# Kernel tuning notes

Measured on AMD Instinct MI355X. Metric: run time of the kernel, lower is better.

## Reference

```python
import jax, jax.numpy as jnp
import numpy as np

MODEL_DIM = 1024
HEADS = 16
HEAD_DIM = MODEL_DIM // HEADS
OUT_DIM = 1024
B, S = 2, 2048


def setup_inputs() -> dict:
    key = jax.random.key(0)
    ks = jax.random.split(key, 10)
    scale = 1.0 / np.sqrt(MODEL_DIM)
    return {
        "query": jax.random.normal(ks[0], (B, S, MODEL_DIM), dtype=jnp.float32),
        "bank": jax.random.normal(ks[1], (B, S, MODEL_DIM), dtype=jnp.float32),
        "Wq": jax.random.normal(ks[2], (MODEL_DIM, MODEL_DIM), dtype=jnp.float32) * scale,
        "bq": jnp.zeros((MODEL_DIM,), dtype=jnp.float32),
        "Wk": jax.random.normal(ks[3], (MODEL_DIM, MODEL_DIM), dtype=jnp.float32) * scale,
        "bk": jnp.zeros((MODEL_DIM,), dtype=jnp.float32),
        "Wv": jax.random.normal(ks[4], (MODEL_DIM, MODEL_DIM), dtype=jnp.float32) * scale,
        "bv": jnp.zeros((MODEL_DIM,), dtype=jnp.float32),
        "Wo": jax.random.normal(ks[5], (OUT_DIM, MODEL_DIM), dtype=jnp.float32) * scale,
        "bo": jnp.zeros((OUT_DIM,), dtype=jnp.float32),
    }


def _split_heads(x):
    # [B, S, D] -> [B, H, S, hd]
    b, s, _ = x.shape
    return x.reshape(b, s, HEADS, HEAD_DIM).transpose(0, 2, 1, 3)


def reference(query, bank, Wq, bq, Wk, bk, Wv, bv, Wo, bo):
    # Linear projections (torch Linear: x @ W.T + b)
    q = _split_heads(query @ Wq.T + bq)  # [B,H,Sq,hd]
    k = _split_heads(bank @ Wk.T + bk)   # [B,H,Sk,hd]
    v = _split_heads(bank @ Wv.T + bv)   # [B,H,Sk,hd]
    score_scale = jnp.sqrt(jnp.float32(HEAD_DIM))
    scores = jnp.einsum("bhqd,bhkd->bhqk", q / score_scale, k)  # [B,H,Sq,Sk]
    attn = jax.nn.softmax(scores, axis=-1)
    # dropout is identity in eval-mode reference
    ctx = jnp.einsum("bhqk,bhkd->bhqd", attn, v)  # [B,H,Sq,hd]
    b, h, sq, hd = ctx.shape
    ctx = ctx.transpose(0, 2, 1, 3).reshape(b, sq, MODEL_DIM)
    return ctx @ Wo.T + bo
```

## Files before the change

kernel.cpp:

```cpp
#include <hip/hip_runtime.h>


#define BDIM   2
#define SDIM   2048
#define DDIM   1024
#define HEADS  16
#define HD     64
#define MROWS  (BDIM * SDIM)

typedef float  f32x4  __attribute__((ext_vector_type(4)));
typedef __bf16 bf16x8 __attribute__((ext_vector_type(8)));
typedef __bf16 bf16x4 __attribute__((ext_vector_type(4)));

#define QSCALE 0.18033688011112042f

__device__ __forceinline__ void stage16(const void* g, void* l) {
    __builtin_amdgcn_global_load_lds((const __attribute__((address_space(1))) void*)g,
                                     (__attribute__((address_space(3))) void*)l,
                                     16, 0, 0);
}

__global__ __launch_bounds__(256) void cvt8(const float* __restrict__ in,
                                            __bf16* __restrict__ out, int n8) {
    int i = blockIdx.x * 256 + threadIdx.x;
    if (i >= n8) return;
    const float4* p = (const float4*)in;
    float4 a = p[2 * i];
    float4 c = p[2 * i + 1];
    bf16x8 o;
    o[0] = (__bf16)a.x; o[1] = (__bf16)a.y; o[2] = (__bf16)a.z; o[3] = (__bf16)a.w;
    o[4] = (__bf16)c.x; o[5] = (__bf16)c.y; o[6] = (__bf16)c.z; o[7] = (__bf16)c.w;
    *(bf16x8*)(out + 8 * i) = o;
}

__global__ __launch_bounds__(256) void cvt8w(const float* __restrict__ w0,
                                             const float* __restrict__ w1,
                                             const float* __restrict__ w2,
                                             const float* __restrict__ w3,
                                             __bf16* __restrict__ o0,
                                             __bf16* __restrict__ o1,
                                             __bf16* __restrict__ o2,
                                             __bf16* __restrict__ o3) {
    const int sel = blockIdx.x >> 9;
    const float* in  = (sel == 0) ? w0 : (sel == 1) ? w1 : (sel == 2) ? w2 : w3;
    __bf16*      out = (sel == 0) ? o0 : (sel == 1) ? o1 : (sel == 2) ? o2 : o3;
    int i = (blockIdx.x & 511) * 256 + threadIdx.x;
    const float4* p = (const float4*)in;
    float4 a = p[2 * i];
    float4 c = p[2 * i + 1];
    bf16x8 o;
    o[0] = (__bf16)a.x; o[1] = (__bf16)a.y; o[2] = (__bf16)a.z; o[3] = (__bf16)a.w;
    o[4] = (__bf16)c.x; o[5] = (__bf16)c.y; o[6] = (__bf16)c.z; o[7] = (__bf16)c.w;
    *(bf16x8*)(out + 8 * i) = o;
}

template <bool QKV>
__global__ __launch_bounds__(256) void gemm_bt(
    const __bf16* __restrict__ Aq, const __bf16* __restrict__ Akv,
    const __bf16* __restrict__ W0, const __bf16* __restrict__ W1,
    const __bf16* __restrict__ W2,
    const float* __restrict__ b0, const float* __restrict__ b1,
    const float* __restrict__ b2,
    __bf16* __restrict__ Qo, __bf16* __restrict__ Ko, __bf16* __restrict__ Vo,
    float* __restrict__ Fo) {
    __shared__ __align__(16) __bf16 ldsA[128 * 32];
    __shared__ __align__(16) __bf16 ldsB[128 * 32];

    const int t = threadIdx.x;
    const int l = t & 63;
    const int w = t >> 6;
    const int z = QKV ? (int)blockIdx.z : 0;

    const __bf16* A  = (QKV && z != 0) ? Akv : Aq;
    const __bf16* Wm = (z == 0) ? W0 : (z == 1 ? W1 : W2);
    const float*  bias = (z == 0) ? b0 : (z == 1 ? b1 : b2);

    const int row0 = blockIdx.y * 128;
    const int col0 = blockIdx.x * 128;

    const __bf16* ga = A  + (size_t)(row0 + (t >> 2)) * DDIM + (t & 3) * 8;
    const __bf16* gb = Wm + (size_t)(col0 + (t >> 2)) * DDIM + (t & 3) * 8;
    __bf16* la = ldsA + (t & ~63) * 8;
    __bf16* lb = ldsB + (t & ~63) * 8;

    const int wm = w >> 1, wn = w & 1;
    const int aoff = (wm * 64 + (l & 15)) * 32 + (l >> 4) * 8;
    const int boff = (wn * 64 + (l & 15)) * 32 + (l >> 4) * 8;

    f32x4 acc[4][4] = {};

    for (int kb = 0; kb < DDIM; kb += 32) {
        __syncthreads();
        stage16(ga + kb,             la);
        stage16(ga + kb + 64 * DDIM, la + 2048);
        stage16(gb + kb,             lb);
        stage16(gb + kb + 64 * DDIM, lb + 2048);
        __syncthreads();

        bf16x8 af[4], bf[4];
#pragma unroll
        for (int m = 0; m < 4; ++m) af[m] = *(const bf16x8*)(ldsA + aoff + m * 16 * 32);
#pragma unroll
        for (int n = 0; n < 4; ++n) bf[n] = *(const bf16x8*)(ldsB + boff + n * 16 * 32);
#pragma unroll
        for (int m = 0; m < 4; ++m)
#pragma unroll
            for (int n = 0; n < 4; ++n)
                acc[m][n] = __builtin_amdgcn_mfma_f32_16x16x32_bf16(af[m], bf[n], acc[m][n], 0, 0, 0);
    }

#pragma unroll
    for (int m = 0; m < 4; ++m) {
        const int rbase = row0 + wm * 64 + m * 16 + (l >> 4) * 4;
#pragma unroll
        for (int n = 0; n < 4; ++n) {
            const int col = col0 + wn * 64 + n * 16 + (l & 15);
            const float bv = bias[col];
            if constexpr (QKV) {
                const int hh = col >> 6, d = col & 63;
#pragma unroll
                for (int j = 0; j < 4; ++j) {
                    const int r = rbase + j;
                    const int b = r >> 11, s = r & 2047;
                    const float v = acc[m][n][j] + bv;
                    if (z == 0) {
                        Qo[(((b * HEADS + hh) * SDIM + s) << 6) + d] = (__bf16)(v * QSCALE);
                    } else if (z == 1) {
                        Ko[(((b * HEADS + hh) * SDIM + s) << 6) + d] = (__bf16)v;
                    } else {
                        Vo[(((b * HEADS + hh) * HD + d) << 11) + s] = (__bf16)v;
                    }
                }
            } else {
#pragma unroll
                for (int j = 0; j < 4; ++j) {
                    Fo[(size_t)(rbase + j) * DDIM + col] = acc[m][n][j] + bv;
                }
            }
        }
    }
}

__global__ __launch_bounds__(512) void attn_fwd(const __bf16* __restrict__ Qb,
                                                const __bf16* __restrict__ Kb,
                                                const __bf16* __restrict__ Vtb,
                                                __bf16* __restrict__ Cb) {
    __shared__ __align__(16) __bf16 ldsK[2][2][64 * 64];
    __shared__ __align__(16) __bf16 ldsV[2][2][64 * 64];

    const int t = threadIdx.x;
    const int l = t & 63;
    const int w = t >> 6;
    const int i15 = l & 15;
    const int q4 = l >> 4;

    const int bid  = blockIdx.x;
    const int xcd  = bid & 7;
    const int wloc = bid >> 3;
    const int bh   = xcd * 4 + (wloc >> 4);
    const int qb   = wloc & 15;
    const int b    = bh >> 4;
    const int h    = bh & 15;
    const size_t base = (size_t)bh * SDIM * HD;
    const int q0 = qb * 128;

    const __bf16* qp = Qb + base + (size_t)(q0 + w * 16 + i15) * HD + q4 * 8;
    const bf16x8 qf0 = *(const bf16x8*)(qp);
    const bf16x8 qf1 = *(const bf16x8*)(qp + 32);

    const int r0 = t >> 3;
    const int sl = (t & 7) ^ (r0 & 7);
    const int sig0 = ((r0 >> 5) << 5) | (((r0 >> 2) & 3) << 3)
                   | (((r0 >> 4) & 1) << 2) | (r0 & 3);
    const __bf16* gk = Kb  + base + (size_t)sig0 * HD + sl * 8;
    const __bf16* gv = Vtb + base + (size_t)r0 * SDIM + sl * 8;
    const int wb = (t & ~63) * 8;

    const int xr = i15 & 7;
    int off[4][2];
#pragma unroll
    for (int n = 0; n < 4; ++n)
#pragma unroll
        for (int hh = 0; hh < 2; ++hh)
            off[n][hh] = (n * 16 + i15) * 64 + (((hh * 4 + q4) ^ xr) << 3);

    bf16x8 ones;
#pragma unroll
    for (int j = 0; j < 8; ++j) ones[j] = (__bf16)1.0f;

    f32x4 c[4] = {};
    f32x4 lsum = {};

    stage16(gk,           &ldsK[0][0][wb]);
    stage16(gk + 64 * HD, &ldsK[0][1][wb]);
    stage16(gv,           &ldsV[0][0][wb]);
    stage16(gv + 64,      &ldsV[0][1][wb]);

    for (int r = 0; r < SDIM / 128; ++r) {
        const int bb = r & 1;
        __syncthreads();

        if (r + 1 < SDIM / 128) {
            const int s0 = (r + 1) * 128;
            stage16(gk + (size_t)s0 * HD,        &ldsK[bb ^ 1][0][wb]);
            stage16(gk + (size_t)(s0 + 64) * HD, &ldsK[bb ^ 1][1][wb]);
            stage16(gv + s0,                     &ldsV[bb ^ 1][0][wb]);
            stage16(gv + s0 + 64,                &ldsV[bb ^ 1][1][wb]);
        }

        const __bf16* lk0 = &ldsK[bb][0][0];
        const __bf16* lk1 = &ldsK[bb][1][0];
        const __bf16* lv0 = &ldsV[bb][0][0];
        const __bf16* lv1 = &ldsV[bb][1][0];

        f32x4 sA[4] = {}, sB[4] = {};
        __builtin_amdgcn_s_setprio(1);
#pragma unroll
        for (int n = 0; n < 4; ++n) {
            bf16x8 k0 = *(const bf16x8*)(lk0 + off[n][0]);
            bf16x8 k1 = *(const bf16x8*)(lk0 + off[n][1]);
            sA[n] = __builtin_amdgcn_mfma_f32_16x16x32_bf16(k0, qf0, sA[n], 0, 0, 0);
            sA[n] = __builtin_amdgcn_mfma_f32_16x16x32_bf16(k1, qf1, sA[n], 0, 0, 0);
        }
#pragma unroll
        for (int n = 0; n < 4; ++n) {
            bf16x8 k0 = *(const bf16x8*)(lk1 + off[n][0]);
            bf16x8 k1 = *(const bf16x8*)(lk1 + off[n][1]);
            sB[n] = __builtin_amdgcn_mfma_f32_16x16x32_bf16(k0, qf0, sB[n], 0, 0, 0);
            sB[n] = __builtin_amdgcn_mfma_f32_16x16x32_bf16(k1, qf1, sB[n], 0, 0, 0);
        }
        __builtin_amdgcn_s_setprio(0);

#pragma unroll
        for (int n = 0; n < 4; ++n)
#pragma unroll
            for (int j = 0; j < 4; ++j) {
                sA[n][j] = exp2f(sA[n][j]);
                sB[n][j] = exp2f(sB[n][j]);
            }

        bf16x8 paA0, paB0, paA1, paB1;
#pragma unroll
        for (int j = 0; j < 4; ++j) {
            paA0[j]     = (__bf16)sA[0][j];
            paA0[j + 4] = (__bf16)sA[1][j];
            paB0[j]     = (__bf16)sA[2][j];
            paB0[j + 4] = (__bf16)sA[3][j];
            paA1[j]     = (__bf16)sB[0][j];
            paA1[j + 4] = (__bf16)sB[1][j];
            paB1[j]     = (__bf16)sB[2][j];
            paB1[j + 4] = (__bf16)sB[3][j];
        }

        __builtin_amdgcn_s_setprio(1);
        lsum = __builtin_amdgcn_mfma_f32_16x16x32_bf16(ones, paA0, lsum, 0, 0, 0);
        lsum = __builtin_amdgcn_mfma_f32_16x16x32_bf16(ones, paB0, lsum, 0, 0, 0);
        lsum = __builtin_amdgcn_mfma_f32_16x16x32_bf16(ones, paA1, lsum, 0, 0, 0);
        lsum = __builtin_amdgcn_mfma_f32_16x16x32_bf16(ones, paB1, lsum, 0, 0, 0);
#pragma unroll
        for (int n2 = 0; n2 < 4; ++n2) {
            bf16x8 v0 = *(const bf16x8*)(lv0 + off[n2][0]);
            bf16x8 v1 = *(const bf16x8*)(lv0 + off[n2][1]);
            c[n2] = __builtin_amdgcn_mfma_f32_16x16x32_bf16(v0, paA0, c[n2], 0, 0, 0);
            c[n2] = __builtin_amdgcn_mfma_f32_16x16x32_bf16(v1, paB0, c[n2], 0, 0, 0);
            bf16x8 u0 = *(const bf16x8*)(lv1 + off[n2][0]);
            bf16x8 u1 = *(const bf16x8*)(lv1 + off[n2][1]);
            c[n2] = __builtin_amdgcn_mfma_f32_16x16x32_bf16(u0, paA1, c[n2], 0, 0, 0);
            c[n2] = __builtin_amdgcn_mfma_f32_16x16x32_bf16(u1, paB1, c[n2], 0, 0, 0);
        }
        __builtin_amdgcn_s_setprio(0);
    }

    const float inv = 1.0f / lsum[0];
    const int q = q0 + w * 16 + i15;
#pragma unroll
    for (int n2 = 0; n2 < 4; ++n2) {
        bf16x4 o;
#pragma unroll
        for (int j = 0; j < 4; ++j) o[j] = (__bf16)(c[n2][j] * inv);
        *(bf16x4*)(Cb + (size_t)(b * SDIM + q) * DDIM + h * HD + n2 * 16 + q4 * 4) = o;
    }
}

extern "C" void kernel_launch(void* const* d_in, const int* in_sizes, int n_in,
                              void* d_out, int out_size, void* d_ws, size_t ws_size,
                              hipStream_t stream) {
    const float* query = (const float*)d_in[0];
    const float* bank  = (const float*)d_in[1];
    const float* Wq = (const float*)d_in[2];
    const float* bq = (const float*)d_in[3];
    const float* Wk = (const float*)d_in[4];
    const float* bk = (const float*)d_in[5];
    const float* Wv = (const float*)d_in[6];
    const float* bv = (const float*)d_in[7];
    const float* Wo = (const float*)d_in[8];
    const float* bo = (const float*)d_in[9];
    float* out = (float*)d_out;

    char* ws = (char*)d_ws;
    __bf16* xq  = (__bf16*)(ws);
    __bf16* xkv = (__bf16*)(ws + (8u  << 20));
    __bf16* wq  = (__bf16*)(ws + (16u << 20));
    __bf16* wk  = (__bf16*)(ws + (18u << 20));
    __bf16* wv  = (__bf16*)(ws + (20u << 20));
    __bf16* wo  = (__bf16*)(ws + (22u << 20));
    __bf16* qbuf = (__bf16*)(ws + (24u << 20));
    __bf16* kbuf = (__bf16*)(ws + (32u << 20));
    __bf16* vtbuf = (__bf16*)(ws + (40u << 20));
    __bf16* ctx = xq;

    cvt8<<<2048, 256, 0, stream>>>(query, xq, 524288);
    cvt8<<<2048, 256, 0, stream>>>(bank, xkv, 524288);
    cvt8w<<<2048, 256, 0, stream>>>(Wq, Wk, Wv, Wo, wq, wk, wv, wo);

    gemm_bt<true><<<dim3(8, 32, 3), 256, 0, stream>>>(
        xq, xkv, wq, wk, wv, bq, bk, bv, qbuf, kbuf, vtbuf, nullptr);

    attn_fwd<<<512, 512, 0, stream>>>(qbuf, kbuf, vtbuf, ctx);

    gemm_bt<false><<<dim3(8, 32, 1), 256, 0, stream>>>(
        ctx, nullptr, wo, nullptr, nullptr, bo, nullptr, nullptr,
        nullptr, nullptr, nullptr, out);
}
```

Baseline: 139.1 us.

## Double-buffer GEMM LDS staging and compute V transposed via swapped operands

Adds double-buffered LDS tiles to the bf16 GEMM so the next K-slice is loaded asynchronously while MFMAs run on the current one, with one barrier per step instead of two. It also splits the V projection into its own launch that computes Wv·X^T directly, so the transposed V layout is written with contiguous sequence-index stores rather than strided scatter. The cost is twice the LDS per block, which may lower occupancy, plus one extra kernel launch.

Result: slower. 159.6 us (+14.7%).

```diff
diff --git a/kernel.cpp b/kernel.cpp
--- a/kernel.cpp
+++ b/kernel.cpp
@@ -54,34 +54,31 @@
     *(bf16x8*)(out + 8 * i) = o;
 }
 
-template <bool QKV>
+template <int MODE>
 __global__ __launch_bounds__(256) void gemm_bt(
     const __bf16* __restrict__ Aq, const __bf16* __restrict__ Akv,
     const __bf16* __restrict__ W0, const __bf16* __restrict__ W1,
-    const __bf16* __restrict__ W2,
     const float* __restrict__ b0, const float* __restrict__ b1,
-    const float* __restrict__ b2,
     __bf16* __restrict__ Qo, __bf16* __restrict__ Ko, __bf16* __restrict__ Vo,
     float* __restrict__ Fo) {
-    __shared__ __align__(16) __bf16 ldsA[128 * 32];
-    __shared__ __align__(16) __bf16 ldsB[128 * 32];
+    __shared__ __align__(16) __bf16 ldsA[2][128 * 32];
+    __shared__ __align__(16) __bf16 ldsB[2][128 * 32];
 
     const int t = threadIdx.x;
     const int l = t & 63;
     const int w = t >> 6;
-    const int z = QKV ? (int)blockIdx.z : 0;
-
-    const __bf16* A  = (QKV && z != 0) ? Akv : Aq;
-    const __bf16* Wm = (z == 0) ? W0 : (z == 1 ? W1 : W2);
-    const float*  bias = (z == 0) ? b0 : (z == 1 ? b1 : b2);
+    const int z = (MODE == 0) ? (int)blockIdx.z : 0;
+
+    const __bf16* A  = (MODE == 0 && z != 0) ? Akv : Aq;
+    const __bf16* Wm = (z == 0) ? W0 : W1;
+    const float*  bias = (z == 0) ? b0 : b1;
 
     const int row0 = blockIdx.y * 128;
     const int col0 = blockIdx.x * 128;
 
     const __bf16* ga = A  + (size_t)(row0 + (t >> 2)) * DDIM + (t & 3) * 8;
     const __bf16* gb = Wm + (size_t)(col0 + (t >> 2)) * DDIM + (t & 3) * 8;
-    __bf16* la = ldsA + (t & ~63) * 8;
-    __bf16* lb = ldsB + (t & ~63) * 8;
+    const int lboff = (t & ~63) * 8;
 
     const int wm = w >> 1, wn = w & 1;
     const int aoff = (wm * 64 + (l & 15)) * 32 + (l >> 4) * 8;
@@ -89,19 +86,28 @@
 
     f32x4 acc[4][4] = {};
 
-    for (int kb = 0; kb < DDIM; kb += 32) {
+    stage16(ga,             &ldsA[0][lboff]);
+    stage16(ga + 64 * DDIM, &ldsA[0][lboff + 2048]);
+    stage16(gb,             &ldsB[0][lboff]);
+    stage16(gb + 64 * DDIM, &ldsB[0][lboff + 2048]);
+
+    for (int step = 0; step < DDIM / 32; ++step) {
+        const int bb = step & 1;
         __syncthreads();
-        stage16(ga + kb,             la);
-        stage16(ga + kb + 64 * DDIM, la + 2048);
-        stage16(gb + kb,             lb);
-        stage16(gb + kb + 64 * DDIM, lb + 2048);
-        __syncthreads();
+
+        if (step + 1 < DDIM / 32) {
+            const int kb = (step + 1) * 32;
+            stage16(ga + kb,             &ldsA[bb ^ 1][lboff]);
+            stage16(ga + kb + 64 * DDIM, &ldsA[bb ^ 1][lboff + 2048]);
+            stage16(gb + kb,             &ldsB[bb ^ 1][lboff]);
+            stage16(gb + kb + 64 * DDIM, &ldsB[bb ^ 1][lboff + 2048]);
+        }
 
         bf16x8 af[4], bf[4];
 #pragma unroll
-        for (int m = 0; m < 4; ++m) af[m] = *(const bf16x8*)(ldsA + aoff + m * 16 * 32);
-#pragma unroll
-        for (int n = 0; n < 4; ++n) bf[n] = *(const bf16x8*)(ldsB + boff + n * 16 * 32);
+        for (int m = 0; m < 4; ++m) af[m] = *(const bf16x8*)(&ldsA[bb][aoff + m * 16 * 32]);
+#pragma unroll
+        for (int n = 0; n < 4; ++n) bf[n] = *(const bf16x8*)(&ldsB[bb][boff + n * 16 * 32]);
 #pragma unroll
         for (int m = 0; m < 4; ++m)
 #pragma unroll
@@ -115,8 +121,8 @@
 #pragma unroll
         for (int n = 0; n < 4; ++n) {
             const int col = col0 + wn * 64 + n * 16 + (l & 15);
-            const float bv = bias[col];
-            if constexpr (QKV) {
+            if constexpr (MODE == 0) {
+                const float bv = bias[col];
                 const int hh = col >> 6, d = col & 63;
 #pragma unroll
                 for (int j = 0; j < 4; ++j) {
@@ -125,13 +131,19 @@
                     const float v = acc[m][n][j] + bv;
                     if (z == 0) {
                         Qo[(((b * HEADS + hh) * SDIM + s) << 6) + d] = (__bf16)(v * QSCALE);
-                    } else if (z == 1) {
+                    } else {
                         Ko[(((b * HEADS + hh) * SDIM + s) << 6) + d] = (__bf16)v;
-                    } else {
-                        Vo[(((b * HEADS + hh) * HD + d) << 11) + s] = (__bf16)v;
                     }
                 }
+            } else if constexpr (MODE == 1) {
+                const int b = col >> 11, s = col & 2047;
+#pragma unroll
+                for (int j = 0; j < 4; ++j) {
+                    const int f = rbase + j;
+                    Vo[(size_t)(b * DDIM + f) * SDIM + s] = (__bf16)(acc[m][n][j] + bias[f]);
+                }
             } else {
+                const float bv = bias[col];
 #pragma unroll
                 for (int j = 0; j < 4; ++j) {
                     Fo[(size_t)(rbase + j) * DDIM + col] = acc[m][n][j] + bv;
@@ -313,12 +325,14 @@
     cvt8<<<2048, 256, 0, stream>>>(bank, xkv, 524288);
     cvt8w<<<2048, 256, 0, stream>>>(Wq, Wk, Wv, Wo, wq, wk, wv, wo);
 
-    gemm_bt<true><<<dim3(8, 32, 3), 256, 0, stream>>>(
-        xq, xkv, wq, wk, wv, bq, bk, bv, qbuf, kbuf, vtbuf, nullptr);
+    gemm_bt<0><<<dim3(8, 32, 2), 256, 0, stream>>>(
+        xq, xkv, wq, wk, bq, bk, qbuf, kbuf, nullptr, nullptr);
+
+    gemm_bt<1><<<dim3(32, 8, 1), 256, 0, stream>>>(
+        wv, nullptr, xkv, nullptr, bv, nullptr, nullptr, nullptr, vtbuf, nullptr);
 
     attn_fwd<<<512, 512, 0, stream>>>(qbuf, kbuf, vtbuf, ctx);
 
-    gemm_bt<false><<<dim3(8, 32, 1), 256, 0, stream>>>(
-        ctx, nullptr, wo, nullptr, nullptr, bo, nullptr, nullptr,
-        nullptr, nullptr, nullptr, out);
-}
+    gemm_bt<2><<<dim3(8, 32, 1), 256, 0, stream>>>(
+        ctx, nullptr, wo, nullptr, bo, nullptr, nullptr, nullptr, nullptr, out);
+}
```
